# Performance work log

Measured on AMD Instinct MI355X. Metric: run time of the kernel, lower is better.

Reference implementation:

```python
import jax, jax.numpy as jnp
import numpy as np

N_HEADS = 16
ROPE_BASE = 10000.0


def _rope_tables(T, Dh, dtype):
    # inv_freq over even indices of head_dim, per RotaryEmbedding
    inv_freq = 1.0 / (ROPE_BASE ** (jnp.arange(0, Dh, 2, dtype=jnp.float32) / Dh))
    freqs = jnp.outer(jnp.arange(T, dtype=jnp.float32), inv_freq)  # [T, Dh/2]
    emb = jnp.concatenate([freqs, freqs], axis=-1)                  # [T, Dh]
    return emb.astype(dtype).reshape(1, 1, T, Dh), None


def _rotate_half(x):
    x1, x2 = jnp.split(x, 2, axis=-1)
    return jnp.concatenate([-x2, x1], axis=-1)


def setup_inputs() -> dict:
    key = jax.random.key(0)
    k1, k2, k3 = jax.random.split(key, 3)
    B, T, C = 2, 2048, 1024
    x = jax.random.normal(k1, (B, T, C), dtype=jnp.float32)
    w_qkv = jax.random.normal(k2, (C, 3 * C), dtype=jnp.float32) * (1.0 / np.sqrt(C))
    w_out = jax.random.normal(k3, (C, C), dtype=jnp.float32) * (1.0 / np.sqrt(C))
    return {"x": x, "w_qkv": w_qkv, "w_out": w_out}


def reference(x, w_qkv, w_out):
    B, T, C = x.shape
    H = N_HEADS
    Dh = C // H
    qkv = x @ w_qkv                                   # [B, T, 3C]
    q, k, v = jnp.split(qkv, 3, axis=-1)
    # [B, T, C] -> [B, H, T, Dh]
    def to_heads(t):
        return t.reshape(B, T, H, Dh).transpose(0, 2, 1, 3)
    q, k, v = to_heads(q), to_heads(k), to_heads(v)

    # RoPE
    emb, _ = _rope_tables(T, Dh, x.dtype)             # [1,1,T,Dh] angle table
    cos, sin = jnp.cos(emb), jnp.sin(emb)
    q = q * cos + _rotate_half(q) * sin
    k = k * cos + _rotate_half(k) * sin

    # causal SDPA (eval mode -> no dropout)
    scale = 1.0 / jnp.sqrt(jnp.asarray(Dh, dtype=x.dtype))
    scores = jnp.einsum('bhqd,bhkd->bhqk', q, k) * scale
    causal_mask = jnp.tril(jnp.ones((T, T), dtype=bool))
    scores = jnp.where(causal_mask, scores, jnp.asarray(-jnp.inf, dtype=scores.dtype))
    attn = jax.nn.softmax(scores, axis=-1)
    out = jnp.einsum('bhqk,bhkd->bhqd', attn, v)      # [B,H,T,Dh]
    out = out.transpose(0, 2, 1, 3).reshape(B, T, C)
    return out @ w_out
```

## Files before the change

### kernel.cpp

```cpp
#include <hip/hip_runtime.h>
#include <stdint.h>


typedef __attribute__((ext_vector_type(8))) __bf16 bf16x8;
typedef __attribute__((ext_vector_type(4))) __bf16 bf16x4;
typedef __attribute__((ext_vector_type(4))) float f32x4;

#define MFMA16(a, b, c) __builtin_amdgcn_mfma_f32_16x16x32_bf16((a), (b), (c), 0, 0, 0)

#define SWAIT_VM0()                                     \
    do {                                                \
        asm volatile("s_waitcnt vmcnt(0)" ::: "memory");\
        __builtin_amdgcn_sched_barrier(0);              \
    } while (0)
#define SWAIT_LGKM0()                                     \
    do {                                                  \
        asm volatile("s_waitcnt lgkmcnt(0)" ::: "memory");\
        __builtin_amdgcn_sched_barrier(0);                \
    } while (0)

__device__ __forceinline__ void gl_lds16(const void* g, void* l) {
    __builtin_amdgcn_global_load_lds(
        (const __attribute__((address_space(1))) void*)g,
        (__attribute__((address_space(3))) void*)l, 16, 0, 0);
}

__device__ __forceinline__ unsigned short f2bf(float f) {
    union { float f; unsigned u; } x; x.f = f;
    unsigned r = x.u + 0x7FFFu + ((x.u >> 16) & 1u);
    return (unsigned short)(r >> 16);
}
__device__ __forceinline__ float bf2f(unsigned short h) {
    union { unsigned u; float f; } x; x.u = ((unsigned)h) << 16;
    return x.f;
}

__global__ void cast_f32_bf16(const float* __restrict__ src,
                              unsigned short* __restrict__ dst, int n4) {
    int i = blockIdx.x * 256 + threadIdx.x;
    if (i >= n4) return;
    float4 v = ((const float4*)src)[i];
    ushort4 o;
    o.x = f2bf(v.x); o.y = f2bf(v.y); o.z = f2bf(v.z); o.w = f2bf(v.w);
    ((ushort4*)dst)[i] = o;
}

__global__ void transpose_cast(const float* __restrict__ src,
                               unsigned short* __restrict__ dst, int K, int N) {
    __shared__ float tile[32][33];
    int n0 = blockIdx.x * 32, k0 = blockIdx.y * 32;
    int r = threadIdx.x >> 5, c = threadIdx.x & 31;
#pragma unroll
    for (int i = 0; i < 4; i++) {
        int kk = r + i * 8;
        tile[kk][c] = src[(size_t)(k0 + kk) * N + n0 + c];
    }
    __syncthreads();
#pragma unroll
    for (int i = 0; i < 4; i++) {
        int nn = r + i * 8;
        dst[(size_t)(n0 + nn) * K + k0 + c] = f2bf(tile[c][nn]);
    }
}

__global__ void rope_tables(float* __restrict__ ct, float* __restrict__ st) {
    int i = blockIdx.x * 256 + threadIdx.x;
    int t = i >> 5, d = i & 31;
    float ex = (float)(2 * d) / 64.0f;
    float inv = powf(10000.0f, -ex);
    float a = (float)t * inv;
    ct[i] = cosf(a);
    st[i] = sinf(a);
}

__global__ void rope_apply(unsigned short* __restrict__ q,
                           unsigned short* __restrict__ k,
                           const float* __restrict__ ct,
                           const float* __restrict__ st) {
    const float QSC = 0.125f * 1.44269504f;
    int i = blockIdx.x * 256 + threadIdx.x;
    int d = i & 31;
    int t = (i >> 5) & 2047;
    int bh = i >> 16;
    size_t base = ((size_t)bh * 2048 + t) * 64;
    float c = ct[t * 32 + d], s = st[t * 32 + d];
    float q1 = bf2f(q[base + d]), q2 = bf2f(q[base + d + 32]);
    q[base + d]      = f2bf((q1 * c - q2 * s) * QSC);
    q[base + d + 32] = f2bf((q2 * c + q1 * s) * QSC);
    float k1 = bf2f(k[base + d]), k2 = bf2f(k[base + d + 32]);
    k[base + d]      = f2bf(k1 * c - k2 * s);
    k[base + d + 32] = f2bf(k2 * c + k1 * s);
}

template <int MODE>
__global__ __launch_bounds__(256) void gemm_bt(
    const unsigned short* __restrict__ A,
    const unsigned short* __restrict__ Bt,
    unsigned short* __restrict__ oq,
    unsigned short* __restrict__ ok,
    unsigned short* __restrict__ ovt,
    float* __restrict__ of,
    int M_, int N_, int K_) {
    __shared__ __attribute__((aligned(16))) unsigned short ldsA[128 * 64];
    __shared__ __attribute__((aligned(16))) unsigned short ldsB[128 * 64];
    const int tid = threadIdx.x;
    const int lane = tid & 63, wv = tid >> 6;
    const int wr = wv >> 1, wc = wv & 1;
    const int l15 = lane & 15, lg = lane >> 4;
    const int lrow = lane >> 3, lch = lane & 7;
    const int swz = (lch * 16) ^ (lrow << 4);
    const int m0 = blockIdx.x * 128, n0 = blockIdx.y * 128;
    const char* Ab = (const char*)A;
    const char* Bb = (const char*)Bt;
    const size_t rstride = (size_t)K_ * 2;

    f32x4 acc[4][4] = {};

    const int nkt = K_ >> 6;
    for (int kt = 0; kt < nkt; kt++) {
        if (kt) __syncthreads();
#pragma unroll
        for (int ii = 0; ii < 4; ii++) {
            int r0 = wv * 32 + ii * 8;
            gl_lds16(Ab + (size_t)(m0 + r0 + lrow) * rstride + kt * 128 + swz,
                     (char*)ldsA + r0 * 128);
            gl_lds16(Bb + (size_t)(n0 + r0 + lrow) * rstride + kt * 128 + swz,
                     (char*)ldsB + r0 * 128);
        }
        __syncthreads();
#pragma unroll
        for (int ks = 0; ks < 2; ks++) {
            const int kb = ks * 64 + lg * 16;
            bf16x8 af[4], bfr[4];
#pragma unroll
            for (int mf = 0; mf < 4; mf++) {
                int row = wr * 64 + mf * 16 + l15;
                af[mf] = *(const bf16x8*)((const char*)ldsA + row * 128 +
                                          (kb ^ ((row & 7) << 4)));
            }
#pragma unroll
            for (int nf = 0; nf < 4; nf++) {
                int row = wc * 64 + nf * 16 + l15;
                bfr[nf] = *(const bf16x8*)((const char*)ldsB + row * 128 +
                                           (kb ^ ((row & 7) << 4)));
            }
#pragma unroll
            for (int mf = 0; mf < 4; mf++)
#pragma unroll
                for (int nf = 0; nf < 4; nf++)
                    acc[mf][nf] = MFMA16(af[mf], bfr[nf], acc[mf][nf]);
        }
    }

#pragma unroll
    for (int mf = 0; mf < 4; mf++) {
#pragma unroll
        for (int nf = 0; nf < 4; nf++) {
#pragma unroll
            for (int j = 0; j < 4; j++) {
                int grow = m0 + wr * 64 + mf * 16 + lg * 4 + j;
                int gcol = n0 + wc * 64 + nf * 16 + l15;
                float v = acc[mf][nf][j];
                if (MODE == 0) {
                    int b = grow >> 11, t = grow & 2047;
                    int s = gcol >> 10, c = gcol & 1023;
                    int h = c >> 6, d = c & 63;
                    int hb = b * 16 + h;
                    unsigned short bv = f2bf(v);
                    if (s == 0)
                        oq[((size_t)hb * 2048 + t) * 64 + d] = bv;
                    else if (s == 1)
                        ok[((size_t)hb * 2048 + t) * 64 + d] = bv;
                    else
                        ovt[((size_t)hb * 64 + d) * 2048 + t] = bv;
                } else {
                    of[(size_t)grow * N_ + gcol] = v;
                }
            }
        }
    }
}

__global__ __launch_bounds__(256, 2) void attn_fwd(
    const unsigned short* __restrict__ Q,
    const unsigned short* __restrict__ K,
    const unsigned short* __restrict__ Vt,
    unsigned short* __restrict__ O) {
    __shared__ __attribute__((aligned(16))) char ldsKV[4][16384];
    __shared__ __attribute__((aligned(16))) char ldsP[4][4096];
    const int tid = threadIdx.x, lane = tid & 63, wv = tid >> 6;
    const int l15 = lane & 15, lg = lane >> 4;
    const int lrow = lane >> 3, lch = lane & 7;
    const int swz = (lch * 16) ^ (lrow << 4);

    const int wg = blockIdx.x;
    const int sz = (wg & 7) * 64 + (wg >> 3);
    const int i = sz & 15, bh = sz >> 4;
    const int b = bh >> 4, h = bh & 15;
    const int wp = (wv + (i & 3)) & 3;
    const int jt = (wp == 0) ? i : (wp == 1) ? (63 - i) : (wp == 2) ? (31 - i)
                                                                    : (32 + i);
    const int q0 = jt * 32;
    const int nkt = (jt >> 1) + 1;

    char* Kb = ldsKV[wv];
    char* Vb = ldsKV[wv] + 8192;
    char* Pb = ldsP[wv];
    const unsigned short* Qh = Q + (size_t)bh * 2048 * 64;
    const char* Kg = (const char*)(K + (size_t)bh * 2048 * 64);
    const char* Vg = (const char*)(Vt + (size_t)bh * 64 * 2048);

    bf16x8 qa[2][2];
#pragma unroll
    for (int mf = 0; mf < 2; mf++)
#pragma unroll
        for (int ks = 0; ks < 2; ks++)
            qa[mf][ks] = *(const bf16x8*)(Qh + (size_t)(q0 + mf * 16 + l15) * 64 +
                                          ks * 32 + lg * 8);

    auto stage = [&](int k0) {
        const char* kg = Kg + (size_t)k0 * 128;
        const char* vg = Vg + (size_t)k0 * 2;
#pragma unroll
        for (int ii = 0; ii < 8; ii++) {
            gl_lds16(kg + (ii * 8 + lrow) * 128 + swz, Kb + ii * 1024);
            gl_lds16(vg + (size_t)(ii * 8 + lrow) * 4096 + swz, Vb + ii * 1024);
        }
    };

    f32x4 oacc[2][4] = {};
    float mi[2] = {-1e30f, -1e30f}, li[2] = {0.f, 0.f};

    stage(0);
    for (int kt = 0; kt < nkt; kt++) {
        const int k0 = kt * 64;
        SWAIT_VM0();
        bf16x8 kb[2][4], vb[2][4];
#pragma unroll
        for (int ks = 0; ks < 2; ks++)
#pragma unroll
            for (int nf = 0; nf < 4; nf++) {
                int row = nf * 16 + l15;
                kb[ks][nf] = *(const bf16x8*)(
                    Kb + row * 128 + ((ks * 64 + lg * 16) ^ ((row & 7) << 4)));
            }
#pragma unroll
        for (int ks = 0; ks < 2; ks++)
#pragma unroll
            for (int df = 0; df < 4; df++) {
                int row = df * 16 + l15;
                vb[ks][df] = *(const bf16x8*)(
                    Vb + row * 128 + ((ks * 64 + lg * 16) ^ ((row & 7) << 4)));
            }
        f32x4 s[2][4] = {};
#pragma unroll
        for (int ks = 0; ks < 2; ks++)
#pragma unroll
            for (int mf = 0; mf < 2; mf++)
#pragma unroll
                for (int nf = 0; nf < 4; nf++)
                    s[mf][nf] = MFMA16(kb[ks][nf], qa[mf][ks], s[mf][nf]);
        SWAIT_LGKM0();
        if (kt + 1 < nkt) stage(k0 + 64);
        const bool dm = (kt == nkt - 1);
#pragma unroll
        for (int mf = 0; mf < 2; mf++) {
            if (dm) {
                int qrow = q0 + mf * 16 + l15;
#pragma unroll
                for (int nf = 0; nf < 4; nf++)
#pragma unroll
                    for (int j = 0; j < 4; j++)
                        if (k0 + nf * 16 + lg * 4 + j > qrow)
                            s[mf][nf][j] = -1e30f;
            }
            float rmax = -1e30f;
#pragma unroll
            for (int nf = 0; nf < 4; nf++)
#pragma unroll
                for (int j = 0; j < 4; j++) rmax = fmaxf(rmax, s[mf][nf][j]);
            rmax = fmaxf(rmax, __shfl_xor(rmax, 16));
            rmax = fmaxf(rmax, __shfl_xor(rmax, 32));
            const float mnew = fmaxf(mi[mf], rmax);
            const float alpha = exp2f(mi[mf] - mnew);
            mi[mf] = mnew;
            float rsum = 0.f;
#pragma unroll
            for (int nf = 0; nf < 4; nf++) {
#pragma unroll
                for (int j = 0; j < 4; j++) {
                    float p = exp2f(s[mf][nf][j] - mnew);
                    s[mf][nf][j] = p;
                    rsum += p;
                }
            }
            rsum += __shfl_xor(rsum, 16);
            rsum += __shfl_xor(rsum, 32);
            li[mf] = li[mf] * alpha + rsum;
#pragma unroll
            for (int nf = 0; nf < 4; nf++) {
                bf16x4 pk;
#pragma unroll
                for (int j = 0; j < 4; j++) pk[j] = (__bf16)s[mf][nf][j];
                int row = mf * 16 + l15;
                *(bf16x4*)(Pb + row * 128 +
                           ((nf * 32 + lg * 8) ^ ((row & 7) << 4))) = pk;
            }
#pragma unroll
            for (int j = 0; j < 4; j++) {
                float aj = __shfl(alpha, lg * 4 + j);
#pragma unroll
                for (int df = 0; df < 4; df++) oacc[mf][df][j] *= aj;
            }
        }
#pragma unroll
        for (int ks = 0; ks < 2; ks++) {
            bf16x8 pa[2];
#pragma unroll
            for (int mf = 0; mf < 2; mf++) {
                int row = mf * 16 + l15;
                pa[mf] = *(const bf16x8*)(
                    Pb + row * 128 + ((ks * 64 + lg * 16) ^ ((row & 7) << 4)));
            }
#pragma unroll
            for (int mf = 0; mf < 2; mf++)
#pragma unroll
                for (int df = 0; df < 4; df++)
                    oacc[mf][df] = MFMA16(pa[mf], vb[ks][df], oacc[mf][df]);
        }
    }
#pragma unroll
    for (int mf = 0; mf < 2; mf++)
#pragma unroll
        for (int j = 0; j < 4; j++) {
            float lj = __shfl(li[mf], lg * 4 + j);
            float rl = 1.0f / lj;
            int t = q0 + mf * 16 + lg * 4 + j;
#pragma unroll
            for (int df = 0; df < 4; df++) {
                int d = df * 16 + l15;
                O[((size_t)(b * 2048 + t)) * 1024 + h * 64 + d] =
                    f2bf(oacc[mf][df][j] * rl);
            }
        }
}

extern "C" void kernel_launch(void* const* d_in, const int* in_sizes, int n_in,
                              void* d_out, int out_size, void* d_ws, size_t ws_size,
                              hipStream_t stream) {
    const float* x     = (const float*)d_in[0];
    const float* w_qkv = (const float*)d_in[1];
    const float* w_out = (const float*)d_in[2];
    float* out = (float*)d_out;
    char* ws = (char*)d_ws;
    const size_t MB = 1024 * 1024;

    unsigned short* xb    = (unsigned short*)(ws);
    unsigned short* wqkvt = (unsigned short*)(ws + 8 * MB);
    unsigned short* woutt = (unsigned short*)(ws + 14 * MB);
    unsigned short* qh    = (unsigned short*)(ws + 16 * MB);
    unsigned short* kh    = (unsigned short*)(ws + 24 * MB);
    unsigned short* vt    = (unsigned short*)(ws + 32 * MB);
    unsigned short* ao    = (unsigned short*)(ws + 40 * MB);
    float* ctab = (float*)(ws + 48 * MB);
    float* stab = (float*)(ws + 48 * MB + 256 * 1024);

    cast_f32_bf16<<<4096, 256, 0, stream>>>(x, xb, (4096 * 1024) / 4);
    transpose_cast<<<dim3(96, 32), 256, 0, stream>>>(w_qkv, wqkvt, 1024, 3072);
    transpose_cast<<<dim3(32, 32), 256, 0, stream>>>(w_out, woutt, 1024, 1024);
    rope_tables<<<256, 256, 0, stream>>>(ctab, stab);

    gemm_bt<0><<<dim3(32, 24), 256, 0, stream>>>(xb, wqkvt, qh, kh, vt, nullptr,
                                                 4096, 3072, 1024);
    rope_apply<<<8192, 256, 0, stream>>>(qh, kh, ctab, stab);
    attn_fwd<<<512, 256, 0, stream>>>(qh, kh, vt, ao);
    gemm_bt<1><<<dim3(32, 8), 256, 0, stream>>>(ao, woutt, nullptr, nullptr,
                                                nullptr, out, 4096, 1024, 1024);
}
```

Measured before the change: 148.0 us.

## Fuse RoPE into QKV GEMM epilogue and split-K attention across two waves

Removes the separate rope_apply kernel by applying the rotation and Q scaling in the QKV GEMM epilogue, using an interleaved cos/sin table. The attention kernel is restructured: 128-thread blocks where two waves split each query tile's KV range and merge partial softmax state through LDS. K/V are now read directly from global into registers with a one-tile prefetch instead of LDS staging. It also adds lazy rescaling (skip the max update unless it grows by more than a threshold) and MFMA priority hints. Risks include uncoalesced direct loads, a bf16-rounded partial output in the merge, and the grid ordering by heaviest tiles first.

New measurement: 187.7 us. 1.27x slower.

```diff
diff --git a/kernel.cpp b/kernel.cpp
--- a/kernel.cpp
+++ b/kernel.cpp
@@ -7,17 +7,6 @@
 typedef __attribute__((ext_vector_type(4))) float f32x4;
 
 #define MFMA16(a, b, c) __builtin_amdgcn_mfma_f32_16x16x32_bf16((a), (b), (c), 0, 0, 0)
-
-#define SWAIT_VM0()                                     \
-    do {                                                \
-        asm volatile("s_waitcnt vmcnt(0)" ::: "memory");\
-        __builtin_amdgcn_sched_barrier(0);              \
-    } while (0)
-#define SWAIT_LGKM0()                                     \
-    do {                                                  \
-        asm volatile("s_waitcnt lgkmcnt(0)" ::: "memory");\
-        __builtin_amdgcn_sched_barrier(0);                \
-    } while (0)
 
 __device__ __forceinline__ void gl_lds16(const void* g, void* l) {
     __builtin_amdgcn_global_load_lds(
@@ -33,6 +22,12 @@
 __device__ __forceinline__ float bf2f(unsigned short h) {
     union { unsigned u; float f; } x; x.u = ((unsigned)h) << 16;
     return x.f;
+}
+__device__ __forceinline__ f32x4 fmax4(f32x4 a, f32x4 b) {
+    f32x4 r;
+#pragma unroll
+    for (int i = 0; i < 4; i++) r[i] = fmaxf(a[i], b[i]);
+    return r;
 }
 
 __global__ void cast_f32_bf16(const float* __restrict__ src,
@@ -63,33 +58,12 @@
     }
 }
 
-__global__ void rope_tables(float* __restrict__ ct, float* __restrict__ st) {
-    int i = blockIdx.x * 256 + threadIdx.x;
-    int t = i >> 5, d = i & 31;
-    float ex = (float)(2 * d) / 64.0f;
-    float inv = powf(10000.0f, -ex);
+__global__ void rope_tables(float2* __restrict__ cst) {
+    int idx = blockIdx.x * 256 + threadIdx.x;
+    int t = idx >> 5, d = idx & 31;
+    float inv = powf(10000.0f, -(float)(2 * d) / 64.0f);
     float a = (float)t * inv;
-    ct[i] = cosf(a);
-    st[i] = sinf(a);
-}
-
-__global__ void rope_apply(unsigned short* __restrict__ q,
-                           unsigned short* __restrict__ k,
-                           const float* __restrict__ ct,
-                           const float* __restrict__ st) {
-    const float QSC = 0.125f * 1.44269504f;
-    int i = blockIdx.x * 256 + threadIdx.x;
-    int d = i & 31;
-    int t = (i >> 5) & 2047;
-    int bh = i >> 16;
-    size_t base = ((size_t)bh * 2048 + t) * 64;
-    float c = ct[t * 32 + d], s = st[t * 32 + d];
-    float q1 = bf2f(q[base + d]), q2 = bf2f(q[base + d + 32]);
-    q[base + d]      = f2bf((q1 * c - q2 * s) * QSC);
-    q[base + d + 32] = f2bf((q2 * c + q1 * s) * QSC);
-    float k1 = bf2f(k[base + d]), k2 = bf2f(k[base + d + 32]);
-    k[base + d]      = f2bf(k1 * c - k2 * s);
-    k[base + d + 32] = f2bf(k2 * c + k1 * s);
+    cst[idx] = make_float2(cosf(a), sinf(a));
 }
 
 template <int MODE>
@@ -100,6 +74,7 @@
     unsigned short* __restrict__ ok,
     unsigned short* __restrict__ ovt,
     float* __restrict__ of,
+    const float2* __restrict__ cst,
     int M_, int N_, int K_) {
     __shared__ __attribute__((aligned(16))) unsigned short ldsA[128 * 64];
     __shared__ __attribute__((aligned(16))) unsigned short ldsB[128 * 64];
@@ -152,63 +127,91 @@
         }
     }
 
-#pragma unroll
-    for (int mf = 0; mf < 4; mf++) {
-#pragma unroll
-        for (int nf = 0; nf < 4; nf++) {
-#pragma unroll
-            for (int j = 0; j < 4; j++) {
-                int grow = m0 + wr * 64 + mf * 16 + lg * 4 + j;
-                int gcol = n0 + wc * 64 + nf * 16 + l15;
-                float v = acc[mf][nf][j];
-                if (MODE == 0) {
+    if (MODE == 0) {
+        const int sblk = n0 >> 10;
+        if (sblk == 2) {
+#pragma unroll
+            for (int mf = 0; mf < 4; mf++)
+#pragma unroll
+                for (int nf = 0; nf < 4; nf++)
+#pragma unroll
+                    for (int j = 0; j < 4; j++) {
+                        int grow = m0 + wr * 64 + mf * 16 + lg * 4 + j;
+                        int gcol = n0 + wc * 64 + nf * 16 + l15;
+                        int b = grow >> 11, t = grow & 2047;
+                        int c = gcol & 1023;
+                        int h = c >> 6, d = c & 63;
+                        int hb = b * 16 + h;
+                        ovt[((size_t)hb * 64 + d) * 2048 + t] =
+                            f2bf(acc[mf][nf][j]);
+                    }
+        } else {
+            const float QSC = 0.125f * 1.44269504f;
+            unsigned short* dst = (sblk == 0) ? oq : ok;
+#pragma unroll
+            for (int mf = 0; mf < 4; mf++)
+#pragma unroll
+                for (int j = 0; j < 4; j++) {
+                    int grow = m0 + wr * 64 + mf * 16 + lg * 4 + j;
                     int b = grow >> 11, t = grow & 2047;
-                    int s = gcol >> 10, c = gcol & 1023;
-                    int h = c >> 6, d = c & 63;
-                    int hb = b * 16 + h;
-                    unsigned short bv = f2bf(v);
-                    if (s == 0)
-                        oq[((size_t)hb * 2048 + t) * 64 + d] = bv;
-                    else if (s == 1)
-                        ok[((size_t)hb * 2048 + t) * 64 + d] = bv;
-                    else
-                        ovt[((size_t)hb * 64 + d) * 2048 + t] = bv;
-                } else {
-                    of[(size_t)grow * N_ + gcol] = v;
-                }
-            }
+#pragma unroll
+                    for (int nf = 0; nf < 2; nf++) {
+                        int gcol = n0 + wc * 64 + nf * 16 + l15;
+                        int c = gcol & 1023;
+                        int h = c >> 6;
+                        int d = nf * 16 + l15;
+                        int hb = b * 16 + h;
+                        float2 csv = cst[t * 32 + d];
+                        float x1 = acc[mf][nf][j];
+                        float x2 = acc[mf][nf + 2][j];
+                        float r1 = x1 * csv.x - x2 * csv.y;
+                        float r2 = x2 * csv.x + x1 * csv.y;
+                        if (sblk == 0) { r1 *= QSC; r2 *= QSC; }
+                        size_t base = ((size_t)hb * 2048 + t) * 64;
+                        dst[base + d] = f2bf(r1);
+                        dst[base + d + 32] = f2bf(r2);
+                    }
+                }
         }
-    }
-}
-
-__global__ __launch_bounds__(256, 2) void attn_fwd(
+    } else {
+#pragma unroll
+        for (int mf = 0; mf < 4; mf++)
+#pragma unroll
+            for (int nf = 0; nf < 4; nf++)
+#pragma unroll
+                for (int j = 0; j < 4; j++) {
+                    int grow = m0 + wr * 64 + mf * 16 + lg * 4 + j;
+                    int gcol = n0 + wc * 64 + nf * 16 + l15;
+                    of[(size_t)grow * N_ + gcol] = acc[mf][nf][j];
+                }
+    }
+}
+
+__global__ __launch_bounds__(128, 3) void attn_fwd(
     const unsigned short* __restrict__ Q,
     const unsigned short* __restrict__ K,
     const unsigned short* __restrict__ Vt,
     unsigned short* __restrict__ O) {
-    __shared__ __attribute__((aligned(16))) char ldsKV[4][16384];
-    __shared__ __attribute__((aligned(16))) char ldsP[4][4096];
+    __shared__ __attribute__((aligned(16))) unsigned short Pbuf[2][2048];
+    __shared__ float ml[2][32][2];
     const int tid = threadIdx.x, lane = tid & 63, wv = tid >> 6;
     const int l15 = lane & 15, lg = lane >> 4;
-    const int lrow = lane >> 3, lch = lane & 7;
-    const int swz = (lch * 16) ^ (lrow << 4);
 
     const int wg = blockIdx.x;
-    const int sz = (wg & 7) * 64 + (wg >> 3);
-    const int i = sz & 15, bh = sz >> 4;
-    const int b = bh >> 4, h = bh & 15;
-    const int wp = (wv + (i & 3)) & 3;
-    const int jt = (wp == 0) ? i : (wp == 1) ? (63 - i) : (wp == 2) ? (31 - i)
-                                                                    : (32 + i);
+    const int xcd = wg & 7, r = wg >> 3;
+    const int bh = xcd * 4 + (r & 3);
+    const int jt = 63 - (r >> 2);
     const int q0 = jt * 32;
     const int nkt = (jt >> 1) + 1;
-
-    char* Kb = ldsKV[wv];
-    char* Vb = ldsKV[wv] + 8192;
-    char* Pb = ldsP[wv];
+    const int hA = nkt >> 1;
+    const int kbeg = wv ? hA : 0;
+    const int kend = wv ? nkt : hA;
+    const int b = bh >> 4, h = bh & 15;
+
     const unsigned short* Qh = Q + (size_t)bh * 2048 * 64;
-    const char* Kg = (const char*)(K + (size_t)bh * 2048 * 64);
-    const char* Vg = (const char*)(Vt + (size_t)bh * 64 * 2048);
+    const unsigned short* Kh = K + (size_t)bh * 2048 * 64;
+    const unsigned short* Vh = Vt + (size_t)bh * 64 * 2048;
+    char* Pb = (char*)Pbuf[wv];
 
     bf16x8 qa[2][2];
 #pragma unroll
@@ -218,131 +221,160 @@
             qa[mf][ks] = *(const bf16x8*)(Qh + (size_t)(q0 + mf * 16 + l15) * 64 +
                                           ks * 32 + lg * 8);
 
-    auto stage = [&](int k0) {
-        const char* kg = Kg + (size_t)k0 * 128;
-        const char* vg = Vg + (size_t)k0 * 2;
-#pragma unroll
-        for (int ii = 0; ii < 8; ii++) {
-            gl_lds16(kg + (ii * 8 + lrow) * 128 + swz, Kb + ii * 1024);
-            gl_lds16(vg + (size_t)(ii * 8 + lrow) * 4096 + swz, Vb + ii * 1024);
-        }
-    };
-
     f32x4 oacc[2][4] = {};
     float mi[2] = {-1e30f, -1e30f}, li[2] = {0.f, 0.f};
-
-    stage(0);
-    for (int kt = 0; kt < nkt; kt++) {
-        const int k0 = kt * 64;
-        SWAIT_VM0();
-        bf16x8 kb[2][4], vb[2][4];
-#pragma unroll
-        for (int ks = 0; ks < 2; ks++)
-#pragma unroll
-            for (int nf = 0; nf < 4; nf++) {
-                int row = nf * 16 + l15;
-                kb[ks][nf] = *(const bf16x8*)(
-                    Kb + row * 128 + ((ks * 64 + lg * 16) ^ ((row & 7) << 4)));
+    bf16x8 kb[2][4], vb[2][4];
+
+#define LOADK(K0)                                                             \
+    do {                                                                      \
+        _Pragma("unroll") for (int ks = 0; ks < 2; ks++)                      \
+            _Pragma("unroll") for (int nf = 0; nf < 4; nf++)                  \
+                kb[ks][nf] = *(const bf16x8*)(                                \
+                    Kh + (size_t)((K0) + nf * 16 + l15) * 64 + ks * 32 +      \
+                    lg * 8);                                                  \
+    } while (0)
+#define LOADV(K0)                                                             \
+    do {                                                                      \
+        _Pragma("unroll") for (int ks = 0; ks < 2; ks++)                      \
+            _Pragma("unroll") for (int df = 0; df < 4; df++)                  \
+                vb[ks][df] = *(const bf16x8*)(                                \
+                    Vh + (size_t)(df * 16 + l15) * 2048 + (K0) + ks * 32 +    \
+                    lg * 8);                                                  \
+    } while (0)
+
+    if (kbeg < kend) {
+        LOADK(kbeg * 64);
+        LOADV(kbeg * 64);
+        for (int kt = kbeg; kt < kend; ++kt) {
+            const int k0 = kt * 64;
+            f32x4 s[2][4] = {};
+            __builtin_amdgcn_s_setprio(1);
+#pragma unroll
+            for (int ks = 0; ks < 2; ks++)
+#pragma unroll
+                for (int mf = 0; mf < 2; mf++)
+#pragma unroll
+                    for (int nf = 0; nf < 4; nf++)
+                        s[mf][nf] = MFMA16(kb[ks][nf], qa[mf][ks], s[mf][nf]);
+            __builtin_amdgcn_s_setprio(0);
+            const bool last = (kt == kend - 1);
+            const int kn = (last ? kt : kt + 1) * 64;
+            if (!last) LOADK(kn);
+            const bool maskt = (kt == nkt - 1);
+#pragma unroll
+            for (int mf = 0; mf < 2; mf++) {
+                if (maskt) {
+                    int qrow = q0 + mf * 16 + l15;
+#pragma unroll
+                    for (int nf = 0; nf < 4; nf++)
+#pragma unroll
+                        for (int j = 0; j < 4; j++)
+                            if (k0 + nf * 16 + lg * 4 + j > qrow)
+                                s[mf][nf][j] = -1e30f;
+                }
+                f32x4 t01 = fmax4(s[mf][0], s[mf][1]);
+                f32x4 t23 = fmax4(s[mf][2], s[mf][3]);
+                f32x4 tm = fmax4(t01, t23);
+                float rmax = fmaxf(fmaxf(tm[0], tm[1]), fmaxf(tm[2], tm[3]));
+                if (__any(rmax > mi[mf] + 10.0f)) {
+                    rmax = fmaxf(rmax, __shfl_xor(rmax, 16));
+                    rmax = fmaxf(rmax, __shfl_xor(rmax, 32));
+                    float mnew = fmaxf(mi[mf], rmax);
+                    float alpha = exp2f(mi[mf] - mnew);
+                    mi[mf] = mnew;
+                    li[mf] *= alpha;
+#pragma unroll
+                    for (int j = 0; j < 4; j++) {
+                        float aj = __shfl(alpha, lg * 4 + j);
+#pragma unroll
+                        for (int df = 0; df < 4; df++) oacc[mf][df][j] *= aj;
+                    }
+                }
+#pragma unroll
+                for (int nf = 0; nf < 4; nf++)
+#pragma unroll
+                    for (int j = 0; j < 4; j++)
+                        s[mf][nf][j] = exp2f(s[mf][nf][j] - mi[mf]);
+                f32x4 s01 = s[mf][0] + s[mf][1];
+                f32x4 s23 = s[mf][2] + s[mf][3];
+                f32x4 ss = s01 + s23;
+                float rsum = (ss[0] + ss[1]) + (ss[2] + ss[3]);
+                rsum += __shfl_xor(rsum, 16);
+                rsum += __shfl_xor(rsum, 32);
+                li[mf] += rsum;
+#pragma unroll
+                for (int nf = 0; nf < 4; nf++) {
+                    bf16x4 pk;
+#pragma unroll
+                    for (int j = 0; j < 4; j++) pk[j] = (__bf16)s[mf][nf][j];
+                    int row = mf * 16 + l15;
+                    *(bf16x4*)(Pb + row * 128 +
+                               ((nf * 32 + lg * 8) ^ ((row & 7) << 4))) = pk;
+                }
             }
 #pragma unroll
-        for (int ks = 0; ks < 2; ks++)
-#pragma unroll
-            for (int df = 0; df < 4; df++) {
-                int row = df * 16 + l15;
-                vb[ks][df] = *(const bf16x8*)(
-                    Vb + row * 128 + ((ks * 64 + lg * 16) ^ ((row & 7) << 4)));
+            for (int ks = 0; ks < 2; ks++) {
+                bf16x8 pa[2];
+#pragma unroll
+                for (int mf = 0; mf < 2; mf++) {
+                    int row = mf * 16 + l15;
+                    pa[mf] = *(const bf16x8*)(
+                        Pb + row * 128 + ((ks * 64 + lg * 16) ^ ((row & 7) << 4)));
+                }
+                __builtin_amdgcn_s_setprio(1);
+#pragma unroll
+                for (int mf = 0; mf < 2; mf++)
+#pragma unroll
+                    for (int df = 0; df < 4; df++)
+                        oacc[mf][df] = MFMA16(pa[mf], vb[ks][df], oacc[mf][df]);
+                __builtin_amdgcn_s_setprio(0);
             }
-        f32x4 s[2][4] = {};
-#pragma unroll
-        for (int ks = 0; ks < 2; ks++)
-#pragma unroll
-            for (int mf = 0; mf < 2; mf++)
-#pragma unroll
-                for (int nf = 0; nf < 4; nf++)
-                    s[mf][nf] = MFMA16(kb[ks][nf], qa[mf][ks], s[mf][nf]);
-        SWAIT_LGKM0();
-        if (kt + 1 < nkt) stage(k0 + 64);
-        const bool dm = (kt == nkt - 1);
+            if (!last) LOADV(kn);
+        }
+    }
+#undef LOADK
+#undef LOADV
+
+    if (lg == 0) {
 #pragma unroll
         for (int mf = 0; mf < 2; mf++) {
-            if (dm) {
-                int qrow = q0 + mf * 16 + l15;
-#pragma unroll
-                for (int nf = 0; nf < 4; nf++)
-#pragma unroll
-                    for (int j = 0; j < 4; j++)
-                        if (k0 + nf * 16 + lg * 4 + j > qrow)
-                            s[mf][nf][j] = -1e30f;
+            ml[wv][mf * 16 + l15][0] = mi[mf];
+            ml[wv][mf * 16 + l15][1] = li[mf];
+        }
+    }
+    if (wv == 1) {
+        unsigned short* Pp = Pbuf[1];
+#pragma unroll
+        for (int mf = 0; mf < 2; mf++)
+#pragma unroll
+            for (int df = 0; df < 4; df++)
+#pragma unroll
+                for (int j = 0; j < 4; j++)
+                    Pp[(mf * 16 + lg * 4 + j) * 64 + df * 16 + l15] =
+                        f2bf(oacc[mf][df][j]);
+    }
+    __syncthreads();
+    if (wv == 0) {
+#pragma unroll
+        for (int mf = 0; mf < 2; mf++)
+#pragma unroll
+            for (int j = 0; j < 4; j++) {
+                int row = mf * 16 + lg * 4 + j;
+                float mA = ml[0][row][0], lA = ml[0][row][1];
+                float mB = ml[1][row][0], lB = ml[1][row][1];
+                float m = fmaxf(mA, mB);
+                float fA = exp2f(mA - m), fB = exp2f(mB - m);
+                float rl = 1.0f / (lA * fA + lB * fB);
+                int t = q0 + row;
+#pragma unroll
+                for (int df = 0; df < 4; df++) {
+                    int d = df * 16 + l15;
+                    float ob = bf2f(Pbuf[1][row * 64 + d]);
+                    float val = (oacc[mf][df][j] * fA + ob * fB) * rl;
+                    O[((size_t)(b * 2048 + t)) * 1024 + h * 64 + d] = f2bf(val);
+                }
             }
-            float rmax = -1e30f;
-#pragma unroll
-            for (int nf = 0; nf < 4; nf++)
-#pragma unroll
-                for (int j = 0; j < 4; j++) rmax = fmaxf(rmax, s[mf][nf][j]);
-            rmax = fmaxf(rmax, __shfl_xor(rmax, 16));
-            rmax = fmaxf(rmax, __shfl_xor(rmax, 32));
-            const float mnew = fmaxf(mi[mf], rmax);
-            const float alpha = exp2f(mi[mf] - mnew);
-            mi[mf] = mnew;
-            float rsum = 0.f;
-#pragma unroll
-            for (int nf = 0; nf < 4; nf++) {
-#pragma unroll
-                for (int j = 0; j < 4; j++) {
-                    float p = exp2f(s[mf][nf][j] - mnew);
-                    s[mf][nf][j] = p;
-                    rsum += p;
-                }
-            }
-            rsum += __shfl_xor(rsum, 16);
-            rsum += __shfl_xor(rsum, 32);
-            li[mf] = li[mf] * alpha + rsum;
-#pragma unroll
-            for (int nf = 0; nf < 4; nf++) {
-                bf16x4 pk;
-#pragma unroll
-                for (int j = 0; j < 4; j++) pk[j] = (__bf16)s[mf][nf][j];
-                int row = mf * 16 + l15;
-                *(bf16x4*)(Pb + row * 128 +
-                           ((nf * 32 + lg * 8) ^ ((row & 7) << 4))) = pk;
-            }
-#pragma unroll
-            for (int j = 0; j < 4; j++) {
-                float aj = __shfl(alpha, lg * 4 + j);
-#pragma unroll
-                for (int df = 0; df < 4; df++) oacc[mf][df][j] *= aj;
-            }
-        }
-#pragma unroll
-        for (int ks = 0; ks < 2; ks++) {
-            bf16x8 pa[2];
-#pragma unroll
-            for (int mf = 0; mf < 2; mf++) {
-                int row = mf * 16 + l15;
-                pa[mf] = *(const bf16x8*)(
-                    Pb + row * 128 + ((ks * 64 + lg * 16) ^ ((row & 7) << 4)));
-            }
-#pragma unroll
-            for (int mf = 0; mf < 2; mf++)
-#pragma unroll
-                for (int df = 0; df < 4; df++)
-                    oacc[mf][df] = MFMA16(pa[mf], vb[ks][df], oacc[mf][df]);
-        }
-    }
-#pragma unroll
-    for (int mf = 0; mf < 2; mf++)
-#pragma unroll
-        for (int j = 0; j < 4; j++) {
-            float lj = __shfl(li[mf], lg * 4 + j);
-            float rl = 1.0f / lj;
-            int t = q0 + mf * 16 + lg * 4 + j;
-#pragma unroll
-            for (int df = 0; df < 4; df++) {
-                int d = df * 16 + l15;
-                O[((size_t)(b * 2048 + t)) * 1024 + h * 64 + d] =
-                    f2bf(oacc[mf][df][j] * rl);
-            }
-        }
+    }
 }
 
 extern "C" void kernel_launch(void* const* d_in, const int* in_sizes, int n_in,
@@ -362,18 +394,17 @@
     unsigned short* kh    = (unsigned short*)(ws + 24 * MB);
     unsigned short* vt    = (unsigned short*)(ws + 32 * MB);
     unsigned short* ao    = (unsigned short*)(ws + 40 * MB);
-    float* ctab = (float*)(ws + 48 * MB);
-    float* stab = (float*)(ws + 48 * MB + 256 * 1024);
+    float2* cst = (float2*)(ws + 48 * MB);
 
     cast_f32_bf16<<<4096, 256, 0, stream>>>(x, xb, (4096 * 1024) / 4);
     transpose_cast<<<dim3(96, 32), 256, 0, stream>>>(w_qkv, wqkvt, 1024, 3072);
     transpose_cast<<<dim3(32, 32), 256, 0, stream>>>(w_out, woutt, 1024, 1024);
-    rope_tables<<<256, 256, 0, stream>>>(ctab, stab);
+    rope_tables<<<256, 256, 0, stream>>>(cst);
 
     gemm_bt<0><<<dim3(32, 24), 256, 0, stream>>>(xb, wqkvt, qh, kh, vt, nullptr,
-                                                 4096, 3072, 1024);
-    rope_apply<<<8192, 256, 0, stream>>>(qh, kh, ctab, stab);
-    attn_fwd<<<512, 256, 0, stream>>>(qh, kh, vt, ao);
+                                                 cst, 4096, 3072, 1024);
+    attn_fwd<<<2048, 128, 0, stream>>>(qh, kh, vt, ao);
     gemm_bt<1><<<dim3(32, 8), 256, 0, stream>>>(ao, woutt, nullptr, nullptr,
-                                                nullptr, out, 4096, 1024, 1024);
-}
+                                                nullptr, out, nullptr,
+                                                4096, 1024, 1024);
+}
```
